# Kernel optimization log

Hardware: AMD Instinct MI355X
Metric: run time of the kernel (lower is better)

Reference implementation:

```python
import jax, jax.numpy as jnp
import numpy as np

B, IN, OUT, E, K = 8192, 512, 720, 16, 2
MOE_TEMP = 1.0


def setup_inputs() -> dict:
    key = jax.random.key(0)
    ks = jax.random.split(key, 5)
    s_in = 1.0 / np.sqrt(IN)
    return {
        "x": jax.random.normal(ks[0], (B, IN), dtype=jnp.float32),
        "Wg": jax.random.normal(ks[1], (IN, E), dtype=jnp.float32) * s_in,
        "bg": jax.random.normal(ks[2], (E,), dtype=jnp.float32) * 0.01,
        "We": jax.random.normal(ks[3], (E, IN, OUT), dtype=jnp.float32) * s_in,
        "be": jax.random.normal(ks[4], (E, OUT), dtype=jnp.float32) * 0.01,
    }


def reference(x, Wg, bg, We, be):
    # Gating (eval mode: no noise, divide by temperature)
    gate = (x @ Wg + bg) / MOE_TEMP                      # [B, E]
    topk_vals, topk_idx = jax.lax.top_k(gate, K)          # [B, K]
    gates = jax.nn.softmax(topk_vals, axis=1)             # [B, K]

    # Dense all-expert forward (as the original module computes)
    expert_out = jnp.einsum('bi,eio->beo', x, We) + be    # [B, E, OUT]
    sel = jnp.take_along_axis(expert_out, topk_idx[:, :, None], axis=1)  # [B, K, OUT]
    output = jnp.sum(gates[:, :, None] * sel, axis=1)     # [B, OUT]

    # Load-balancing loss
    probs = jax.nn.softmax(gate, axis=1)                  # [B, E]
    assign = jnp.argmax(gate, axis=1)                     # [B]
    D = jnp.zeros((E,), dtype=gate.dtype).at[assign].add(1.0) / x.shape[0]
    P = jnp.mean(probs, axis=0)
    lb_loss = jnp.sum(D * P) * E
    return output, lb_loss
```

## Files before the change

### kernel.cpp

```cpp
#include <hip/hip_runtime.h>
#include <hip/hip_bf16.h>


#define BATCH 8192
#define IND   512
#define OUTD  720
#define NEXP  16
#define CPAD  16

typedef __attribute__((ext_vector_type(8))) short short8;
typedef __attribute__((ext_vector_type(4))) float floatx4;

__device__ __forceinline__ unsigned short f2bf(float f) {
    union { float f; unsigned u; } v; v.f = f;
    unsigned r = v.u + 0x7FFFu + ((v.u >> 16) & 1u);
    return (unsigned short)(r >> 16);
}
__device__ __forceinline__ float bf2f(unsigned short u) {
    union { unsigned u; float f; } v; v.u = ((unsigned)u) << 16;
    return v.f;
}

__device__ __forceinline__ void gl2lds16(const void* g, void* l) {
    __builtin_amdgcn_global_load_lds(
        (const __attribute__((address_space(1))) void*)g,
        (__attribute__((address_space(3))) void*)l, 16, 0, 0);
}

__global__ __launch_bounds__(256) void prep_kernel(
    const float* __restrict__ x, const float* __restrict__ Wg,
    const float* __restrict__ bg, const float* __restrict__ We,
    int* __restrict__ counts, float* __restrict__ Psum, float* __restrict__ Dsum,
    float* __restrict__ gates, unsigned short* __restrict__ lists,
    int* __restrict__ inv,
    unsigned short* __restrict__ xb, unsigned short* __restrict__ Wt)
{
    __shared__ __align__(16) char smem[35328];
    int tid = threadIdx.x;

    if (blockIdx.x < 512) {
        float* sWg  = (float*)smem;
        float* sg   = sWg + 16 * 516;
        float* Ploc = sg + 16 * 17;
        float* Dloc = Ploc + 16;
        int* cnt_loc  = (int*)(Dloc + 16);
        int* base_loc = cnt_loc + 16;
        int* off_loc  = base_loc + 16;

        if (tid < 16) { Ploc[tid] = 0.f; Dloc[tid] = 0.f; cnt_loc[tid] = 0; off_loc[tid] = 0; }

        int rbase = blockIdx.x * 16;

        const float4* gw4 = (const float4*)Wg;
        #pragma unroll
        for (int j = 0; j < 8; ++j) {
            int f = tid + j * 256;
            float4 v = gw4[f];
            int i  = f >> 2;
            int e0 = (f & 3) * 4;
            sWg[(e0 + 0) * 516 + i] = v.x;
            sWg[(e0 + 1) * 516 + i] = v.y;
            sWg[(e0 + 2) * 516 + i] = v.z;
            sWg[(e0 + 3) * 516 + i] = v.w;
        }

        const float4* gx4 = (const float4*)(x + (size_t)rbase * IND);
        #pragma unroll
        for (int j = 0; j < 4; ++j) {
            int f = tid + j * 256;
            float4 v0 = gx4[2 * f];
            float4 v1 = gx4[2 * f + 1];
            short8 o;
            o[0] = (short)f2bf(v0.x); o[1] = (short)f2bf(v0.y);
            o[2] = (short)f2bf(v0.z); o[3] = (short)f2bf(v0.w);
            o[4] = (short)f2bf(v1.x); o[5] = (short)f2bf(v1.y);
            o[6] = (short)f2bf(v1.z); o[7] = (short)f2bf(v1.w);
            *(short8*)&xb[(size_t)rbase * IND + (size_t)f * 8] = o;
        }
        __syncthreads();

        int r = tid >> 4, e = tid & 15;
        const float4* xr = (const float4*)(x + (size_t)(rbase + r) * IND);
        const float4* wr = (const float4*)&sWg[e * 516];
        float acc = bg[e];
        #pragma unroll 8
        for (int i4 = 0; i4 < 128; ++i4) {
            float4 a = xr[i4], w = wr[i4];
            acc += a.x * w.x + a.y * w.y + a.z * w.z + a.w * w.w;
        }
        sg[r * 17 + e] = acc;
        __syncthreads();

        int i0 = 0, i1 = 0;
        if (tid < 16) {
            int row = rbase + tid;
            float v0 = -1e30f, v1 = -1e30f;
            float g[16];
            #pragma unroll
            for (int ee = 0; ee < 16; ++ee) {
                float v = sg[tid * 17 + ee]; g[ee] = v;
                if (v > v0)      { v1 = v0; i1 = i0; v0 = v; i0 = ee; }
                else if (v > v1) { v1 = v;  i1 = ee; }
            }
            float e1   = expf(v1 - v0);
            float inv2 = 1.f / (1.f + e1);
            gates[row * 2 + 0] = inv2;
            gates[row * 2 + 1] = e1 * inv2;

            float s = 0.f, pr[16];
            #pragma unroll
            for (int ee = 0; ee < 16; ++ee) { pr[ee] = expf(g[ee] - v0); s += pr[ee]; }
            float invs = 1.f / s;
            #pragma unroll
            for (int ee = 0; ee < 16; ++ee) atomicAdd(&Ploc[ee], pr[ee] * invs);
            atomicAdd(&Dloc[i0], 1.f);
            atomicAdd(&cnt_loc[i0], 1);
            atomicAdd(&cnt_loc[i1], 1);
        }
        __syncthreads();

        if (tid < 16) {
            if (cnt_loc[tid] > 0) base_loc[tid] = atomicAdd(&counts[tid * CPAD], cnt_loc[tid]);
            atomicAdd(&Psum[tid * CPAD], Ploc[tid]);
            atomicAdd(&Dsum[tid * CPAD], Dloc[tid]);
        }
        __syncthreads();

        if (tid < 16) {
            int row = rbase + tid;
            int p0 = base_loc[i0] + atomicAdd(&off_loc[i0], 1);
            lists[i0 * BATCH + p0] = (unsigned short)(row << 1);
            inv[row * 2 + 0] = i0 * BATCH + p0;
            int p1 = base_loc[i1] + atomicAdd(&off_loc[i1], 1);
            lists[i1 * BATCH + p1] = (unsigned short)((row << 1) | 1);
            inv[row * 2 + 1] = i1 * BATCH + p1;
        }
    } else {
        float* tile = (float*)smem;
        int t  = blockIdx.x - 512;
        int e  = t / 184;
        int rem = t - e * 184;
        int kb = (rem / 23) * 64;
        int ob = (rem % 23) * 32;
        const float* src = We + (size_t)e * (IND * OUTD);

        #pragma unroll
        for (int p = 0; p < 2; ++p) {
            int f  = tid + p * 256;
            int kk = f >> 3;
            int o4 = f & 7;
            float4 v = make_float4(0.f, 0.f, 0.f, 0.f);
            if (ob + o4 * 4 < OUTD)
                v = *(const float4*)&src[(size_t)(kb + kk) * OUTD + ob + o4 * 4];
            tile[(o4 * 4 + 0) * 69 + kk] = v.x;
            tile[(o4 * 4 + 1) * 69 + kk] = v.y;
            tile[(o4 * 4 + 2) * 69 + kk] = v.z;
            tile[(o4 * 4 + 3) * 69 + kk] = v.w;
        }
        __syncthreads();

        int o  = tid >> 3;
        int k8 = tid & 7;
        if (ob + o < OUTD) {
            const float* sp = &tile[o * 69 + k8 * 8];
            short8 w;
            #pragma unroll
            for (int q = 0; q < 8; ++q) w[q] = (short)f2bf(sp[q]);
            *(short8*)&Wt[(size_t)e * (OUTD * IND) + (size_t)(ob + o) * IND + kb + k8 * 8] = w;
        }
    }
}

__global__ __launch_bounds__(256, 4) void moe_mfma_kernel(
    const unsigned short* __restrict__ xb, const unsigned short* __restrict__ Wt,
    const float* __restrict__ be,
    const int* __restrict__ counts, const float* __restrict__ gates,
    const unsigned short* __restrict__ lists,
    unsigned short* __restrict__ partial, int use_inv)
{
    int e = blockIdx.z;
    int n = counts[e * CPAD];
    int r0 = blockIdx.y * 128;
    if (r0 >= n) return;
    int n0 = blockIdx.x * 96;

    __shared__ unsigned short sAB[14336];
    __shared__ int   srow[128];
    __shared__ float sgw[128];
    __shared__ unsigned short sent[128];

    int tid = threadIdx.x;
    if (tid < 128) {
        int idx = r0 + tid;
        if (idx < n) {
            int ent = lists[e * BATCH + idx];
            srow[tid] = ent >> 1;
            sgw[tid]  = gates[(ent >> 1) * 2 + (ent & 1)];
            sent[tid] = (unsigned short)ent;
        } else { srow[tid] = 0; sgw[tid] = 0.f; sent[tid] = 0; }
    }
    __syncthreads();

    int lane = tid & 63, wave = tid >> 6;
    int lsub = lane >> 3;
    int swz  = (lane & 7) ^ lsub;

    const unsigned short* aglb[4];
    unsigned short* alds[4];
    #pragma unroll
    for (int g = 0; g < 4; ++g) {
        int row = wave * 32 + g * 8 + lsub;
        aglb[g] = xb + (size_t)srow[row] * IND + swz * 8;
        alds[g] = &sAB[(wave * 32 + g * 8) * 64];
    }
    const unsigned short* bglb[3];
    unsigned short* blds[3];
    #pragma unroll
    for (int g = 0; g < 3; ++g) {
        int col = n0 + wave * 24 + g * 8 + lsub;
        if (col >= OUTD) col = 0;
        bglb[g] = Wt + ((size_t)e * OUTD + col) * IND + swz * 8;
        blds[g] = &sAB[8192 + (wave * 24 + g * 8) * 64];
    }

    int l15 = lane & 15, quad = lane >> 4;
    int wm = (wave & 1) * 64, wn = (wave >> 1) * 48;
    int axor = (l15 & 7) * 8;

    floatx4 acc[4][3] = {};

    for (int kt = 0; kt < IND / 64; ++kt) {
        __syncthreads();
        #pragma unroll
        for (int g = 0; g < 4; ++g) gl2lds16(aglb[g] + kt * 64, alds[g]);
        #pragma unroll
        for (int g = 0; g < 3; ++g) gl2lds16(bglb[g] + kt * 64, blds[g]);
        __syncthreads();

        #pragma unroll
        for (int ks = 0; ks < 2; ++ks) {
            int ko = ((ks * 4 + quad) * 8) ^ axor;
            short8 a[4], b[3];
            #pragma unroll
            for (int i = 0; i < 4; ++i) a[i] = *(const short8*)&sAB[(wm + i * 16 + l15) * 64 + ko];
            #pragma unroll
            for (int j = 0; j < 3; ++j) b[j] = *(const short8*)&sAB[8192 + (wn + j * 16 + l15) * 64 + ko];
            #pragma unroll
            for (int i = 0; i < 4; ++i)
                #pragma unroll
                for (int j = 0; j < 3; ++j)
                    acc[i][j] = __builtin_amdgcn_mfma_f32_16x16x32_bf16(a[i], b[j], acc[i][j], 0, 0, 0);
        }
    }

    __syncthreads();
    #pragma unroll
    for (int j = 0; j < 3; ++j) {
        int coll = wn + j * 16 + l15;
        int gcol = n0 + coll;
        float bev = (gcol < OUTD) ? be[e * OUTD + gcol] : 0.f;
        #pragma unroll
        for (int i = 0; i < 4; ++i) {
            #pragma unroll
            for (int rr = 0; rr < 4; ++rr) {
                int rowl = wm + i * 16 + quad * 4 + rr;
                sAB[rowl * 104 + coll] = f2bf(sgw[rowl] * (acc[i][j][rr] + bev));
            }
        }
    }
    __syncthreads();

    #pragma unroll
    for (int p = 0; p < 6; ++p) {
        int c    = tid + p * 256;
        int rowl = c / 12;
        int ch   = c - rowl * 12;
        int gcol = n0 + ch * 8;
        if (gcol < OUTD && r0 + rowl < n) {
            size_t prow = use_inv ? (size_t)(e * BATCH + r0 + rowl)
                                  : (size_t)sent[rowl];
            *(short8*)&partial[prow * OUTD + gcol] = *(const short8*)&sAB[rowl * 104 + ch * 8];
        }
    }
}

__global__ __launch_bounds__(256) void combine_kernel(
    const unsigned short* __restrict__ partial, const int* __restrict__ inv,
    const float* __restrict__ Psum, const float* __restrict__ Dsum,
    float* __restrict__ out, int use_inv)
{
    unsigned f = blockIdx.x * 256 + threadIdx.x;
    unsigned b = f / 180u;
    unsigned o4 = (f - b * 180u) * 4u;
    size_t row0 = use_inv ? (size_t)inv[2u * b]     : (size_t)(2u * b);
    size_t row1 = use_inv ? (size_t)inv[2u * b + 1] : (size_t)(2u * b + 1);
    ushort4 u0 = *(const ushort4*)&partial[row0 * OUTD + o4];
    ushort4 u1 = *(const ushort4*)&partial[row1 * OUTD + o4];
    float4 rv;
    rv.x = bf2f(u0.x) + bf2f(u1.x);
    rv.y = bf2f(u0.y) + bf2f(u1.y);
    rv.z = bf2f(u0.z) + bf2f(u1.z);
    rv.w = bf2f(u0.w) + bf2f(u1.w);
    *(float4*)(out + (size_t)b * OUTD + o4) = rv;

    if (f == 0) {
        float s = 0.f;
        #pragma unroll
        for (int e = 0; e < NEXP; ++e)
            s += (Dsum[e * CPAD] / (float)BATCH) * (Psum[e * CPAD] / (float)BATCH);
        out[(size_t)BATCH * OUTD] = s * (float)NEXP;
    }
}

extern "C" void kernel_launch(void* const* d_in, const int* in_sizes, int n_in,
                              void* d_out, int out_size, void* d_ws, size_t ws_size,
                              hipStream_t stream)
{
    const float* x  = (const float*)d_in[0];
    const float* Wg = (const float*)d_in[1];
    const float* bg = (const float*)d_in[2];
    const float* We = (const float*)d_in[3];
    const float* be = (const float*)d_in[4];
    float* out = (float*)d_out;

    char* ws = (char*)d_ws;
    int*   counts = (int*)ws;
    float* Psum   = (float*)(ws + 1024);
    float* Dsum   = (float*)(ws + 2048);
    float* gates  = (float*)(ws + 4096);
    unsigned short* lists = (unsigned short*)(ws + 4096 + 65536);
    int*   inv    = (int*)(ws + 4096 + 65536 + 262144);
    size_t off_xb = 4096 + 65536 + 262144 + 65536;
    off_xb = (off_xb + 255) & ~(size_t)255;
    unsigned short* xb = (unsigned short*)(ws + off_xb);
    size_t off_wt = off_xb + (size_t)BATCH * IND * 2;
    unsigned short* Wt = (unsigned short*)(ws + off_wt);
    size_t off_pt = off_wt + (size_t)NEXP * OUTD * IND * 2;
    unsigned short* partial = (unsigned short*)(ws + off_pt);
    size_t req_big = off_pt + (size_t)NEXP * BATCH * OUTD * 2;
    int use_inv = (ws_size >= req_big) ? 1 : 0;

    hipMemsetAsync(ws, 0, 4096, stream);

    prep_kernel<<<512 + 2944, 256, 0, stream>>>(x, Wg, bg, We, counts, Psum, Dsum,
                                                gates, lists, inv, xb, Wt);

    dim3 grid(8, 12, NEXP);
    moe_mfma_kernel<<<grid, 256, 0, stream>>>(xb, Wt, be, counts, gates, lists,
                                              partial, use_inv);

    combine_kernel<<<(BATCH * (OUTD / 4)) / 256, 256, 0, stream>>>(partial, inv,
                                                                   Psum, Dsum, out, use_inv);
}
```

Baseline: 154.2 us.

## Replace global atomics in routing with per-block counts, scan and scatter kernels

Gating blocks now write per-block expert counts, P and D partials and packed per-row slot info without any global atomics. A single-block scan kernel builds per-block base offsets and the totals, and a scatter kernel fills the expert lists and inverse map. This removes contended global atomics and the memset, and makes list order deterministic. In exchange it adds two extra kernel launches, including a serial 512-step scan done by 16 threads in one block.

```diff
diff --git a/kernel.cpp b/kernel.cpp
--- a/kernel.cpp
+++ b/kernel.cpp
@@ -7,6 +7,7 @@
 #define OUTD  720
 #define NEXP  16
 #define CPAD  16
+#define NGBLK 512
 
 typedef __attribute__((ext_vector_type(8))) short short8;
 typedef __attribute__((ext_vector_type(4))) float floatx4;
@@ -30,24 +31,19 @@
 __global__ __launch_bounds__(256) void prep_kernel(
     const float* __restrict__ x, const float* __restrict__ Wg,
     const float* __restrict__ bg, const float* __restrict__ We,
-    int* __restrict__ counts, float* __restrict__ Psum, float* __restrict__ Dsum,
-    float* __restrict__ gates, unsigned short* __restrict__ lists,
-    int* __restrict__ inv,
+    float* __restrict__ gates, int* __restrict__ rowinfo,
+    int* __restrict__ cnt_blk, float* __restrict__ Pblk, float* __restrict__ Dblk,
     unsigned short* __restrict__ xb, unsigned short* __restrict__ Wt)
 {
     __shared__ __align__(16) char smem[35328];
     int tid = threadIdx.x;
 
-    if (blockIdx.x < 512) {
-        float* sWg  = (float*)smem;
-        float* sg   = sWg + 16 * 516;
-        float* Ploc = sg + 16 * 17;
-        float* Dloc = Ploc + 16;
-        int* cnt_loc  = (int*)(Dloc + 16);
-        int* base_loc = cnt_loc + 16;
-        int* off_loc  = base_loc + 16;
-
-        if (tid < 16) { Ploc[tid] = 0.f; Dloc[tid] = 0.f; cnt_loc[tid] = 0; off_loc[tid] = 0; }
+    if (blockIdx.x < NGBLK) {
+        float* sWg   = (float*)smem;
+        float* sg    = sWg + 16 * 516;
+        float* smax  = sg + 16 * 17;
+        float* sinv  = smax + 16;
+        int*   sasgn = (int*)(sinv + 16);
 
         int rbase = blockIdx.x * 16;
 
@@ -91,10 +87,9 @@
         sg[r * 17 + e] = acc;
         __syncthreads();
 
-        int i0 = 0, i1 = 0;
         if (tid < 16) {
             int row = rbase + tid;
-            float v0 = -1e30f, v1 = -1e30f;
+            float v0 = -1e30f, v1 = -1e30f; int i0 = 0, i1 = 0;
             float g[16];
             #pragma unroll
             for (int ee = 0; ee < 16; ++ee) {
@@ -107,37 +102,44 @@
             gates[row * 2 + 0] = inv2;
             gates[row * 2 + 1] = e1 * inv2;
 
-            float s = 0.f, pr[16];
-            #pragma unroll
-            for (int ee = 0; ee < 16; ++ee) { pr[ee] = expf(g[ee] - v0); s += pr[ee]; }
-            float invs = 1.f / s;
-            #pragma unroll
-            for (int ee = 0; ee < 16; ++ee) atomicAdd(&Ploc[ee], pr[ee] * invs);
-            atomicAdd(&Dloc[i0], 1.f);
-            atomicAdd(&cnt_loc[i0], 1);
-            atomicAdd(&cnt_loc[i1], 1);
+            float s = 0.f;
+            #pragma unroll
+            for (int ee = 0; ee < 16; ++ee) s += expf(g[ee] - v0);
+            smax[tid]  = v0;
+            sinv[tid]  = 1.f / s;
+            sasgn[tid] = i0 | (i1 << 8);
         }
         __syncthreads();
 
         if (tid < 16) {
-            if (cnt_loc[tid] > 0) base_loc[tid] = atomicAdd(&counts[tid * CPAD], cnt_loc[tid]);
-            atomicAdd(&Psum[tid * CPAD], Ploc[tid]);
-            atomicAdd(&Dsum[tid * CPAD], Dloc[tid]);
-        }
-        __syncthreads();
-
-        if (tid < 16) {
-            int row = rbase + tid;
-            int p0 = base_loc[i0] + atomicAdd(&off_loc[i0], 1);
-            lists[i0 * BATCH + p0] = (unsigned short)(row << 1);
-            inv[row * 2 + 0] = i0 * BATCH + p0;
-            int p1 = base_loc[i1] + atomicAdd(&off_loc[i1], 1);
-            lists[i1 * BATCH + p1] = (unsigned short)((row << 1) | 1);
-            inv[row * 2 + 1] = i1 * BATCH + p1;
+            int me  = sasgn[tid];
+            int i0  = me & 255, i1 = me >> 8;
+            int p0 = 0, p1 = 0;
+            for (int rp = 0; rp < tid; ++rp) {
+                int a = sasgn[rp];
+                int a0 = a & 255, a1 = a >> 8;
+                p0 += (a0 == i0) + (a1 == i0);
+                p1 += (a0 == i1) + (a1 == i1);
+            }
+            rowinfo[rbase + tid] = i0 | (i1 << 4) | (p0 << 8) | (p1 << 13);
+
+            int ee = tid;
+            int cnt = 0; float D = 0.f, P = 0.f;
+            #pragma unroll
+            for (int rp = 0; rp < 16; ++rp) {
+                int a = sasgn[rp];
+                int a0 = a & 255, a1 = a >> 8;
+                cnt += (a0 == ee) + (a1 == ee);
+                D   += (a0 == ee) ? 1.f : 0.f;
+                P   += expf(sg[rp * 17 + ee] - smax[rp]) * sinv[rp];
+            }
+            cnt_blk[blockIdx.x * 16 + ee] = cnt;
+            Dblk[blockIdx.x * 16 + ee]    = D;
+            Pblk[blockIdx.x * 16 + ee]    = P;
         }
     } else {
         float* tile = (float*)smem;
-        int t  = blockIdx.x - 512;
+        int t  = blockIdx.x - NGBLK;
         int e  = t / 184;
         int rem = t - e * 184;
         int kb = (rem / 23) * 64;
@@ -169,6 +171,69 @@
             *(short8*)&Wt[(size_t)e * (OUTD * IND) + (size_t)(ob + o) * IND + kb + k8 * 8] = w;
         }
     }
+}
+
+__global__ __launch_bounds__(256) void scan_kernel(
+    const int* __restrict__ cnt_blk, const float* __restrict__ Pblk,
+    const float* __restrict__ Dblk,
+    int* __restrict__ base_blk, int* __restrict__ counts,
+    float* __restrict__ Psum, float* __restrict__ Dsum)
+{
+    __shared__ int scnt[NGBLK * 16];
+    __shared__ float sredP[256], sredD[256];
+    int tid = threadIdx.x;
+
+    #pragma unroll
+    for (int j = 0; j < 32; ++j) scnt[tid + j * 256] = cnt_blk[tid + j * 256];
+    __syncthreads();
+
+    if (tid < 16) {
+        int run = 0;
+        for (int b = 0; b < NGBLK; ++b) {
+            int c = scnt[b * 16 + tid];
+            scnt[b * 16 + tid] = run;
+            run += c;
+        }
+        counts[tid * CPAD] = run;
+    }
+    __syncthreads();
+
+    #pragma unroll
+    for (int j = 0; j < 32; ++j) base_blk[tid + j * 256] = scnt[tid + j * 256];
+
+    int e = tid & 15, stripe = tid >> 4;
+    float accP = 0.f, accD = 0.f;
+    for (int j = 0; j < 32; ++j) {
+        int b = stripe * 32 + j;
+        accP += Pblk[b * 16 + e];
+        accD += Dblk[b * 16 + e];
+    }
+    sredP[tid] = accP; sredD[tid] = accD;
+    __syncthreads();
+    if (tid < 16) {
+        float P = 0.f, D = 0.f;
+        #pragma unroll
+        for (int s = 0; s < 16; ++s) { P += sredP[s * 16 + tid]; D += sredD[s * 16 + tid]; }
+        Psum[tid * CPAD] = P;
+        Dsum[tid * CPAD] = D;
+    }
+}
+
+__global__ __launch_bounds__(256) void scatter_kernel(
+    const int* __restrict__ rowinfo, const int* __restrict__ base_blk,
+    unsigned short* __restrict__ lists, int* __restrict__ inv)
+{
+    int row = blockIdx.x * 256 + threadIdx.x;
+    int info = rowinfo[row];
+    int i0 = info & 15, i1 = (info >> 4) & 15;
+    int p0 = (info >> 8) & 31, p1 = (info >> 13) & 31;
+    int b = row >> 4;
+    int pos0 = base_blk[b * 16 + i0] + p0;
+    int pos1 = base_blk[b * 16 + i1] + p1;
+    lists[i0 * BATCH + pos0] = (unsigned short)(row << 1);
+    lists[i1 * BATCH + pos1] = (unsigned short)((row << 1) | 1);
+    inv[row * 2 + 0] = i0 * BATCH + pos0;
+    inv[row * 2 + 1] = i1 * BATCH + pos1;
 }
 
 __global__ __launch_bounds__(256, 4) void moe_mfma_kernel(
@@ -324,14 +389,18 @@
     float* out = (float*)d_out;
 
     char* ws = (char*)d_ws;
-    int*   counts = (int*)ws;
-    float* Psum   = (float*)(ws + 1024);
-    float* Dsum   = (float*)(ws + 2048);
-    float* gates  = (float*)(ws + 4096);
-    unsigned short* lists = (unsigned short*)(ws + 4096 + 65536);
-    int*   inv    = (int*)(ws + 4096 + 65536 + 262144);
-    size_t off_xb = 4096 + 65536 + 262144 + 65536;
-    off_xb = (off_xb + 255) & ~(size_t)255;
+    int*   counts  = (int*)ws;
+    float* Psum    = (float*)(ws + 1024);
+    float* Dsum    = (float*)(ws + 2048);
+    float* gates   = (float*)(ws + 4096);
+    unsigned short* lists = (unsigned short*)(ws + 69632);
+    int*   inv     = (int*)(ws + 331776);
+    int*   cnt_blk = (int*)(ws + 397312);
+    int*   base_blk= (int*)(ws + 430080);
+    float* Pblk    = (float*)(ws + 462848);
+    float* Dblk    = (float*)(ws + 495616);
+    int*   rowinfo = (int*)(ws + 528384);
+    size_t off_xb  = 561152;
     unsigned short* xb = (unsigned short*)(ws + off_xb);
     size_t off_wt = off_xb + (size_t)BATCH * IND * 2;
     unsigned short* Wt = (unsigned short*)(ws + off_wt);
@@ -340,10 +409,12 @@
     size_t req_big = off_pt + (size_t)NEXP * BATCH * OUTD * 2;
     int use_inv = (ws_size >= req_big) ? 1 : 0;
 
-    hipMemsetAsync(ws, 0, 4096, stream);
-
-    prep_kernel<<<512 + 2944, 256, 0, stream>>>(x, Wg, bg, We, counts, Psum, Dsum,
-                                                gates, lists, inv, xb, Wt);
+    prep_kernel<<<NGBLK + 2944, 256, 0, stream>>>(x, Wg, bg, We, gates, rowinfo,
+                                                  cnt_blk, Pblk, Dblk, xb, Wt);
+
+    scan_kernel<<<1, 256, 0, stream>>>(cnt_blk, Pblk, Dblk, base_blk, counts, Psum, Dsum);
+
+    scatter_kernel<<<BATCH / 256, 256, 0, stream>>>(rowinfo, base_blk, lists, inv);
 
     dim3 grid(8, 12, NEXP);
     moe_mfma_kernel<<<grid, 256, 0, stream>>>(xb, Wt, be, counts, gates, lists,
```

After: 150.7 us. 2.3% less time.
